# Kernel optimization log

Measured on AMD Instinct MI355X. Metric: run time of the kernel, lower is better.

Reference implementation:

```python
import jax, jax.numpy as jnp
import numpy as np

NEG_SLOPE = 0.2  # DGL GATConv default leaky_relu slope


def gat_conv(x, src, dst, W, attn_l, attn_r, bias, res_W):
    """DGL GATConv (eval mode, residual=True with linear res_fc, bias).
    x: [N, F_in]; src/dst: [E]; W: [F_in, H*D]; attn_l/r: [H, D];
    bias: [H*D]; res_W: [F_in, H*D]. Returns [N, H, D]."""
    N = x.shape[0]
    H, D = attn_l.shape
    feat = (x @ W).reshape(N, H, D)
    el = jnp.sum(feat * attn_l, axis=-1)  # [N, H]
    er = jnp.sum(feat * attn_r, axis=-1)  # [N, H]
    e = jax.nn.leaky_relu(el[src] + er[dst], NEG_SLOPE)  # [E, H]
    # edge softmax over incoming edges of each dst node (numerically stable)
    m = jnp.full((N, H), -jnp.inf, dtype=e.dtype).at[dst].max(e)
    ex = jnp.exp(e - m[dst])
    s = jnp.zeros((N, H), dtype=e.dtype).at[dst].add(ex)
    alpha = ex / s[dst]  # [E, H]
    # scatter-aggregate messages alpha * feat[src] into dst
    rst = jnp.zeros((N, H, D), dtype=x.dtype).at[dst].add(alpha[:, :, None] * feat[src])
    rst = rst + (x @ res_W).reshape(N, H, D) + bias.reshape(1, H, D)
    return rst


def setup_inputs() -> dict:
    key = jax.random.key(0)
    N, E, F_IN, HID, OUT, H = 20000, 320000, 128, 128, 128, 4
    ks = jax.random.split(key, 32)
    ki = iter(range(32))

    def rn(shape, scale=0.05):
        return jax.random.normal(ks[next(ki)], shape, dtype=jnp.float32) * scale

    inp = {
        "n_feat": jax.random.normal(ks[next(ki)], (N, F_IN), dtype=jnp.float32),
        "src": jax.random.randint(ks[next(ki)], (E,), 0, N, dtype=jnp.int32),
        "dst": jax.random.randint(ks[next(ki)], (E,), 0, N, dtype=jnp.int32),
        # input GATConv: F_IN -> H x HID
        "W0": rn((F_IN, H * HID)), "al0": rn((H, HID)), "ar0": rn((H, HID)),
        "b0": rn((H * HID,)), "rW0": rn((F_IN, H * HID)),
        "DW0": rn((H * HID, HID)), "Db0": rn((HID,)),
        # middle GATConv: HID -> H x HID
        "W1": rn((HID, H * HID)), "al1": rn((H, HID)), "ar1": rn((H, HID)),
        "b1": rn((H * HID,)), "rW1": rn((HID, H * HID)),
        "DW1": rn((H * HID, HID)), "Db1": rn((HID,)),
        # output GATConv: HID -> H x OUT
        "W2": rn((HID, H * OUT)), "al2": rn((H, OUT)), "ar2": rn((H, OUT)),
        "b2": rn((H * OUT,)), "rW2": rn((HID, H * OUT)),
    }
    return inp


def reference(n_feat, src, dst,
              W0, al0, ar0, b0, rW0, DW0, Db0,
              W1, al1, ar1, b1, rW1, DW1, Db1,
              W2, al2, ar2, b2, rW2):
    N = n_feat.shape[0]
    relu = jax.nn.relu
    # input GAT block
    h = relu(gat_conv(n_feat, src, dst, W0, al0, ar0, b0, rW0))  # [N, H, HID]
    h = relu(h.reshape(N, -1) @ DW0 + Db0)                        # [N, HID]
    # middle GAT block
    h = relu(gat_conv(h, src, dst, W1, al1, ar1, b1, rW1))
    h = relu(h.reshape(N, -1) @ DW1 + Db1)
    # output GAT + head-mean + graph max pooling (single graph)
    h = relu(gat_conv(h, src, dst, W2, al2, ar2, b2, rW2))        # [N, H, OUT]
    h = relu(jnp.mean(h, axis=-2))                                 # [N, OUT]
    return jnp.max(h, axis=0, keepdims=True)                       # [1, OUT]
```

## Files before the change

### kernel.cpp

```cpp
#include <hip/hip_runtime.h>
#include <hip/hip_bf16.h>


typedef __attribute__((ext_vector_type(8))) short bf16x8;
typedef __attribute__((ext_vector_type(4))) float f32x4;
typedef __hip_bfloat16 bf16_t;

#define NEG_SLOPE 0.2f

__device__ __forceinline__ unsigned int pack_bf16(float lo, float hi) {
  return (((unsigned int)__bfloat16_as_ushort(__float2bfloat16(hi))) << 16) |
         (unsigned int)__bfloat16_as_ushort(__float2bfloat16(lo));
}

__device__ __forceinline__ float leaky_exp(float e) {
  e = (e > 0.f) ? e : NEG_SLOPE * e;
  return __expf(e);
}

__device__ __forceinline__ void gload_lds16(const void* g, void* l) {
  __builtin_amdgcn_global_load_lds(
      (const __attribute__((address_space(1))) void*)g,
      (__attribute__((address_space(3))) void*)l, 16, 0, 0);
}

__global__ __launch_bounds__(256) void mega_prep(
    const float* __restrict__ W0, const float* __restrict__ rW0,
    const float* __restrict__ W1, const float* __restrict__ rW1,
    const float* __restrict__ W2, const float* __restrict__ rW2,
    const float* __restrict__ DW0, const float* __restrict__ DW1,
    const float* __restrict__ al0, const float* __restrict__ ar0,
    const float* __restrict__ al1, const float* __restrict__ ar1,
    const float* __restrict__ al2, const float* __restrict__ ar2,
    const float* __restrict__ n_feat, bf16_t* __restrict__ wts,
    float* __restrict__ ALR, bf16_t* __restrict__ xbf,
    int* __restrict__ counts, float* __restrict__ partials, int N) {
  __shared__ float tile[32][33];
  int b = blockIdx.x, tid = threadIdx.x;
  int r = tid >> 5, c = tid & 31;

  if (b < 384) {
    int mat = b >> 6;
    int t = b & 63;
    int kt = t >> 4, nt = t & 15;
    int L = mat >> 1, isR = mat & 1;
    const float* S = (L == 0) ? (isR ? rW0 : W0)
                   : (L == 1) ? (isR ? rW1 : W1) : (isR ? rW2 : W2);
    bf16_t* D = wts + L * 131072 + isR * 65536;
#pragma unroll
    for (int rr = 0; rr < 4; rr++)
      tile[r + rr * 8][c] = S[(kt * 32 + r + rr * 8) * 512 + nt * 32 + c];
    __syncthreads();
#pragma unroll
    for (int rr = 0; rr < 4; rr++)
      D[(nt * 32 + r + rr * 8) * 128 + kt * 32 + c] =
          __float2bfloat16(tile[c][r + rr * 8]);
  } else if (b < 512) {
    int i = b - 384;
    int mat = i >> 6;
    int t = i & 63;
    int kt = t & 15, nt = t >> 4;
    const float* S = mat ? DW1 : DW0;
    bf16_t* D = wts + 393216 + mat * 65536;
#pragma unroll
    for (int rr = 0; rr < 4; rr++)
      tile[r + rr * 8][c] = S[(kt * 32 + r + rr * 8) * 128 + nt * 32 + c];
    __syncthreads();
#pragma unroll
    for (int rr = 0; rr < 4; rr++)
      D[(nt * 32 + r + rr * 8) * 512 + kt * 32 + c] =
          __float2bfloat16(tile[c][r + rr * 8]);
  } else if (b < 524) {
    int idx = (b - 512) * 256 + tid;
    if (idx < 3072) {
      int L = idx >> 10;
      int k = (idx >> 3) & 127;
      int cc = idx & 7;
      int h = cc & 3;
      const float* W = (L == 0) ? W0 : (L == 1) ? W1 : W2;
      const float* a = (cc < 4) ? ((L == 0) ? al0 : (L == 1) ? al1 : al2)
                                : ((L == 0) ? ar0 : (L == 1) ? ar1 : ar2);
      float s = 0.f;
      for (int d = 0; d < 128; d++) s += W[k * 512 + h * 128 + d] * a[h * 128 + d];
      ALR[idx] = s;
    }
  } else if (b < 3024) {
    int i = ((b - 524) * 256 + tid) * 4;
    if (i < N * 128) {
      float4 v = *(const float4*)(n_feat + i);
      xbf[i + 0] = __float2bfloat16(v.x);
      xbf[i + 1] = __float2bfloat16(v.y);
      xbf[i + 2] = __float2bfloat16(v.z);
      xbf[i + 3] = __float2bfloat16(v.w);
    }
  } else {
    for (int i = tid; i < N; i += 256) counts[i] = 0;
    for (int i = tid; i < 64 * 128; i += 256) partials[i] = 0.f;
  }
}

template <bool COUNT>
__global__ __launch_bounds__(256) void gemm128el(
    const bf16_t* __restrict__ A, const bf16_t* __restrict__ Bt,
    const float* __restrict__ ALRl, bf16_t* __restrict__ featB,
    bf16_t* __restrict__ resB,
    float* __restrict__ el, float* __restrict__ er, int M, int K,
    const int* __restrict__ dst, int* __restrict__ counts, int E) {
  __shared__ bf16_t As[128 * 64];
  __shared__ bf16_t Bs[128 * 64];
  int tid = threadIdx.x;
  int rowBase = blockIdx.y * 128;

  if (COUNT && blockIdx.x == 9) {
    int stride = gridDim.y * 256;
    for (int i = blockIdx.y * 256 + tid; i < E; i += stride)
      atomicAdd(&counts[dst[i]], 1);
    return;
  }

  if (blockIdx.x == 8) {
    float* sALR = (float*)As;
#pragma unroll
    for (int j = 0; j < 4; j++) sALR[tid * 4 + j] = ALRl[tid * 4 + j];
    __syncthreads();
    int row = rowBase + (tid >> 1);
    int half = tid & 1;
    if (row < M) {
      const bf16_t* xr = A + (size_t)row * K + half * 64;
      float s[8] = {};
#pragma unroll
      for (int g = 0; g < 8; g++) {
        bf16x8 v = *(const bf16x8*)(xr + g * 8);
#pragma unroll
        for (int e = 0; e < 8; e++) {
          float f = __uint_as_float(((unsigned int)(unsigned short)v[e]) << 16);
          const float* Ak = sALR + (half * 64 + g * 8 + e) * 8;
#pragma unroll
          for (int cc = 0; cc < 8; cc++) s[cc] += f * Ak[cc];
        }
      }
#pragma unroll
      for (int cc = 0; cc < 8; cc++) s[cc] += __shfl_xor(s[cc], 1);
      if (half == 0)
        *(float4*)(el + row * 4) = make_float4(s[0], s[1], s[2], s[3]);
      else
        *(float4*)(er + row * 4) = make_float4(s[4], s[5], s[6], s[7]);
    }
    return;
  }

  int lane = tid & 63, wave = tid >> 6;
  int q = lane >> 4, r16 = lane & 15;
  int wm = (wave >> 1) * 64, wn = (wave & 1) * 64;
  int colBase = blockIdx.x * 128;
  bf16_t* Cb = (colBase < 512) ? featB : resB;
  int colOff = (colBase < 512) ? colBase : colBase - 512;

  f32x4 acc[4][4] = {};

  for (int k0 = 0; k0 < K; k0 += 64) {
#pragma unroll
    for (int p = 0; p < 4; p++) {
      int slotb = (wave * 4 + p) * 64;
      int s = slotb + lane;
      int r = s >> 3;
      int c = (s & 7) ^ (r & 7);
      int gr = rowBase + r;
      if (gr > M - 1) gr = M - 1;
      gload_lds16(A + (size_t)gr * K + k0 + c * 8, (char*)As + (size_t)slotb * 16);
      gload_lds16(Bt + (size_t)(colBase + r) * K + k0 + c * 8,
                  (char*)Bs + (size_t)slotb * 16);
    }
    __syncthreads();
#pragma unroll
    for (int ks = 0; ks < 64; ks += 32) {
      int koff = ks >> 3;
      bf16x8 af[4], bfr[4];
#pragma unroll
      for (int i = 0; i < 4; i++) {
        int R = wm + i * 16 + r16;
        int slot = R * 8 + ((q + koff) ^ (R & 7));
        af[i] = *(const bf16x8*)((const char*)As + (size_t)slot * 16);
      }
#pragma unroll
      for (int j = 0; j < 4; j++) {
        int R = wn + j * 16 + r16;
        int slot = R * 8 + ((q + koff) ^ (R & 7));
        bfr[j] = *(const bf16x8*)((const char*)Bs + (size_t)slot * 16);
      }
#pragma unroll
      for (int i = 0; i < 4; i++)
#pragma unroll
        for (int j = 0; j < 4; j++)
          acc[i][j] = __builtin_amdgcn_mfma_f32_16x16x32_bf16(af[i], bfr[j], acc[i][j], 0, 0, 0);
    }
    __syncthreads();
  }

  int odd = lane & 1;
  int colb0 = r16 & ~1;
#pragma unroll
  for (int i = 0; i < 4; i++) {
#pragma unroll
    for (int r = 0; r < 4; r++) {
      int row = rowBase + wm + i * 16 + q * 4 + r;
#pragma unroll
      for (int jp = 0; jp < 2; jp++) {
        float a0 = acc[i][2 * jp][r];
        float a1 = acc[i][2 * jp + 1][r];
        float p0 = __shfl_xor(a0, 1);
        float p1 = __shfl_xor(a1, 1);
        float lo = odd ? p1 : a0;
        float hi = odd ? a1 : p0;
        int col = colOff + wn + (2 * jp + odd) * 16 + colb0;
        if (row < M)
          *(unsigned int*)(Cb + (size_t)row * 512 + col) = pack_bf16(lo, hi);
      }
    }
  }
}

__global__ __launch_bounds__(256) void mfma_gemm64(
    const bf16_t* __restrict__ A, const bf16_t* __restrict__ Bt,
    const float* __restrict__ bias, bf16_t* __restrict__ C,
    int M, int ldc, int K) {
  __shared__ bf16_t As[64 * 64];
  __shared__ bf16_t Bs[64 * 64];
  int tid = threadIdx.x;
  int lane = tid & 63, wave = tid >> 6;
  int q = lane >> 4, r16 = lane & 15;
  int wm = (wave >> 1) * 32, wn = (wave & 1) * 32;
  int rowBase = blockIdx.y * 64, colBase = blockIdx.x * 64;

  f32x4 acc[2][2] = {};

  for (int k0 = 0; k0 < K; k0 += 64) {
#pragma unroll
    for (int p = 0; p < 2; p++) {
      int slotb = (wave * 2 + p) * 64;
      int s = slotb + lane;
      int r = s >> 3;
      int c = (s & 7) ^ (r & 7);
      int gr = rowBase + r;
      if (gr > M - 1) gr = M - 1;
      gload_lds16(A + (size_t)gr * K + k0 + c * 8, (char*)As + (size_t)slotb * 16);
      gload_lds16(Bt + (size_t)(colBase + r) * K + k0 + c * 8,
                  (char*)Bs + (size_t)slotb * 16);
    }
    __syncthreads();
#pragma unroll
    for (int ks = 0; ks < 64; ks += 32) {
      int koff = ks >> 3;
      bf16x8 af[2], bfr[2];
#pragma unroll
      for (int i = 0; i < 2; i++) {
        int R = wm + i * 16 + r16;
        int slot = R * 8 + ((q + koff) ^ (R & 7));
        af[i] = *(const bf16x8*)((const char*)As + (size_t)slot * 16);
      }
#pragma unroll
      for (int j = 0; j < 2; j++) {
        int R = wn + j * 16 + r16;
        int slot = R * 8 + ((q + koff) ^ (R & 7));
        bfr[j] = *(const bf16x8*)((const char*)Bs + (size_t)slot * 16);
      }
#pragma unroll
      for (int i = 0; i < 2; i++)
#pragma unroll
        for (int j = 0; j < 2; j++)
          acc[i][j] = __builtin_amdgcn_mfma_f32_16x16x32_bf16(af[i], bfr[j], acc[i][j], 0, 0, 0);
    }
    __syncthreads();
  }

  int odd = lane & 1;
  int colb0 = r16 & ~1;
#pragma unroll
  for (int i = 0; i < 2; i++) {
#pragma unroll
    for (int r = 0; r < 4; r++) {
      int row = rowBase + wm + i * 16 + q * 4 + r;
      float a0 = acc[i][0][r];
      float a1 = acc[i][1][r];
      float p0 = __shfl_xor(a0, 1);
      float p1 = __shfl_xor(a1, 1);
      float lo = odd ? p1 : a0;
      float hi = odd ? a1 : p0;
      int col = colBase + wn + odd * 16 + colb0;
      if (row < M) {
        float o0 = fmaxf(lo + bias[col], 0.f);
        float o1 = fmaxf(hi + bias[col + 1], 0.f);
        *(unsigned int*)(C + (size_t)row * ldc + col) = pack_bf16(o0, o1);
      }
    }
  }
}

__global__ __launch_bounds__(1024) void scan_kernel(const int* __restrict__ counts,
                                                    int* __restrict__ row_ptr,
                                                    int* __restrict__ cursor, int N) {
  __shared__ int sums[1024];
  int t = threadIdx.x;
  int chunk = (N + 1023) / 1024;
  int begin = t * chunk;
  int end = begin + chunk;
  if (end > N) end = N;
  int s = 0;
  for (int i = begin; i < end; i++) s += counts[i];
  sums[t] = s;
  __syncthreads();
  for (int off = 1; off < 1024; off <<= 1) {
    int v = (t >= off) ? sums[t - off] : 0;
    __syncthreads();
    sums[t] += v;
    __syncthreads();
  }
  int run = (t == 0) ? 0 : sums[t - 1];
  for (int i = begin; i < end; i++) {
    row_ptr[i] = run;
    cursor[i] = run;
    run += counts[i];
  }
  if (t == 1023) row_ptr[N] = sums[1023];
}

__global__ __launch_bounds__(256) void scatter_w_kernel(
    const int* __restrict__ src, const int* __restrict__ dst,
    int* __restrict__ cursor, int* __restrict__ edge_src,
    int* __restrict__ edge_dst, const float* __restrict__ el,
    const float* __restrict__ er, float* __restrict__ wcsr, int E) {
  int i = blockIdx.x * blockDim.x + threadIdx.x;
  if (i < E) {
    int s = src[i];
    int d = dst[i];
    int pos = atomicAdd(&cursor[d], 1);
    edge_src[pos] = s;
    edge_dst[pos] = d;
    float4 elv = *(const float4*)(el + s * 4);
    float4 erv = *(const float4*)(er + d * 4);
    float4 w;
    w.x = leaky_exp(elv.x + erv.x);
    w.y = leaky_exp(elv.y + erv.y);
    w.z = leaky_exp(elv.z + erv.z);
    w.w = leaky_exp(elv.w + erv.w);
    *(float4*)(wcsr + (size_t)pos * 4) = w;
  }
}

__global__ __launch_bounds__(256) void w_pass_kernel(
    const int* __restrict__ edge_src, const int* __restrict__ edge_dst,
    const float* __restrict__ el, const float* __restrict__ er,
    float* __restrict__ wcsr, int E) {
  int p = blockIdx.x * blockDim.x + threadIdx.x;
  if (p < E) {
    int s = edge_src[p];
    int d = edge_dst[p];
    float4 elv = *(const float4*)(el + s * 4);
    float4 erv = *(const float4*)(er + d * 4);
    float4 w;
    w.x = leaky_exp(elv.x + erv.x);
    w.y = leaky_exp(elv.y + erv.y);
    w.z = leaky_exp(elv.z + erv.z);
    w.w = leaky_exp(elv.w + erv.w);
    *(float4*)(wcsr + (size_t)p * 4) = w;
  }
}

template <bool POOL>
__global__ __launch_bounds__(256) void gat_agg_kernel(
    const bf16_t* __restrict__ featB,
    const bf16_t* __restrict__ resB,
    const float* __restrict__ wcsr,
    const float* __restrict__ bias, const int* __restrict__ row_ptr,
    const int* __restrict__ edge_src, bf16_t* __restrict__ out,
    float* __restrict__ partials, int N) {
  __shared__ float accL[4][64][8];
  __shared__ float ssumL[4][4];
  int n = blockIdx.x;
  int tid = threadIdx.x;
  int wave = tid >> 6, lane = tid & 63;
  int hh = lane >> 4;
  int start = row_ptr[n];
  int deg = row_ptr[n + 1] - start;

  float acc[8] = {};
  float ssum = 0.f;
  const bf16_t* fbase = featB + (size_t)lane * 8;
  for (int i = wave; i < deg; i += 4) {
    int p = start + i;
    int s = edge_src[p];
    float wv = wcsr[(size_t)p * 4 + hh];
    ssum += wv;
    uint4 f = *(const uint4*)(fbase + (size_t)s * 512);
    unsigned int u[4] = {f.x, f.y, f.z, f.w};
#pragma unroll
    for (int j = 0; j < 4; j++) {
      acc[2 * j] += wv * __uint_as_float(u[j] << 16);
      acc[2 * j + 1] += wv * __uint_as_float(u[j] & 0xffff0000u);
    }
  }
  *(float4*)&accL[wave][lane][0] = make_float4(acc[0], acc[1], acc[2], acc[3]);
  *(float4*)&accL[wave][lane][4] = make_float4(acc[4], acc[5], acc[6], acc[7]);
  if ((lane & 15) == 0) ssumL[wave][hh] = ssum;
  __syncthreads();

  int d = tid * 2;
  int l = d >> 3, j = d & 7;
  float a0 = 0.f, a1 = 0.f;
#pragma unroll
  for (int w = 0; w < 4; w++) {
    a0 += accL[w][l][j];
    a1 += accL[w][l][j + 1];
  }
  int h = tid >> 6;
  float ssum4 = ssumL[0][h] + ssumL[1][h] + ssumL[2][h] + ssumL[3][h];
  float inv = (deg > 0) ? 1.f / ssum4 : 0.f;
  unsigned int ru = *(const unsigned int*)(resB + (size_t)n * 512 + d);
  float2 bv = *(const float2*)(bias + d);
  float o0 = fmaxf(a0 * inv + __uint_as_float(ru << 16) + bv.x, 0.f);
  float o1 = fmaxf(a1 * inv + __uint_as_float(ru & 0xffff0000u) + bv.y, 0.f);

  if (!POOL) {
    *(unsigned int*)(out + (size_t)n * 512 + d) = pack_bf16(o0, o1);
  } else {
    float2* red = (float2*)accL;
    __syncthreads();
    red[tid] = make_float2(o0, o1);
    __syncthreads();
    if (tid < 64) {
      float m0 = 0.25f * (red[tid].x + red[tid + 64].x + red[tid + 128].x + red[tid + 192].x);
      float m1 = 0.25f * (red[tid].y + red[tid + 64].y + red[tid + 128].y + red[tid + 192].y);
      float* slot = partials + (n & 63) * 128;
      atomicMax((int*)slot + 2 * tid, __float_as_int(m0));
      atomicMax((int*)slot + 2 * tid + 1, __float_as_int(m1));
    }
  }
}

__global__ __launch_bounds__(128) void pool_finish(const float* __restrict__ partials,
                                                   float* __restrict__ out) {
  int d = threadIdx.x;
  float m = 0.f;
#pragma unroll 8
  for (int s = 0; s < 64; s++) m = fmaxf(m, partials[s * 128 + d]);
  out[d] = m;
}

extern "C" void kernel_launch(void* const* d_in, const int* in_sizes, int n_in,
                              void* d_out, int out_size, void* d_ws, size_t ws_size,
                              hipStream_t stream) {
  const float* n_feat = (const float*)d_in[0];
  const int* src = (const int*)d_in[1];
  const int* dst = (const int*)d_in[2];
  const float* W0 = (const float*)d_in[3];
  const float* al0 = (const float*)d_in[4];
  const float* ar0 = (const float*)d_in[5];
  const float* b0 = (const float*)d_in[6];
  const float* rW0 = (const float*)d_in[7];
  const float* DW0 = (const float*)d_in[8];
  const float* Db0 = (const float*)d_in[9];
  const float* W1 = (const float*)d_in[10];
  const float* al1 = (const float*)d_in[11];
  const float* ar1 = (const float*)d_in[12];
  const float* b1 = (const float*)d_in[13];
  const float* rW1 = (const float*)d_in[14];
  const float* DW1 = (const float*)d_in[15];
  const float* Db1 = (const float*)d_in[16];
  const float* W2 = (const float*)d_in[17];
  const float* al2 = (const float*)d_in[18];
  const float* ar2 = (const float*)d_in[19];
  const float* b2 = (const float*)d_in[20];
  const float* rW2 = (const float*)d_in[21];

  const int N = in_sizes[0] / 128;
  const int E = in_sizes[1];

  bf16_t* xbf = (bf16_t*)d_ws;
  bf16_t* featB = xbf + (size_t)N * 128;
  bf16_t* resB = featB + (size_t)N * 512;
  bf16_t* outC = resB + (size_t)N * 512;
  bf16_t* denseD = outC + (size_t)N * 512;
  bf16_t* wts = denseD + (size_t)N * 128;
  float* ALR = (float*)(wts + 524288);
  float* el = ALR + 3072;
  float* er = el + (size_t)N * 4;
  float* partials = er + (size_t)N * 4;
  float* wcsr = partials + 64 * 128;
  int* counts = (int*)(wcsr + (size_t)E * 4);
  int* row_ptr = counts + N;
  int* cursor = row_ptr + (N + 1);
  int* edge_src = cursor + N;
  int* edge_dst = edge_src + E;

  bf16_t* FW0 = wts;
  bf16_t* FW1 = wts + 131072;
  bf16_t* FW2 = wts + 262144;
  bf16_t* DWt0 = wts + 393216;
  bf16_t* DWt1 = wts + 458752;

  mega_prep<<<3025, 256, 0, stream>>>(
      W0, rW0, W1, rW1, W2, rW2, DW0, DW1,
      al0, ar0, al1, ar1, al2, ar2,
      n_feat, wts, ALR, xbf, counts, partials, N);

  int nRow = (N + 127) / 128;
  dim3 gF0(10, nRow);
  dim3 gF(9, nRow);
  dim3 gD(2, (N + 63) / 64);
  int gE = (E + 255) / 256;

  gemm128el<true><<<gF0, 256, 0, stream>>>(xbf, FW0, ALR, featB, resB, el, er,
                                           N, 128, dst, counts, E);
  scan_kernel<<<1, 1024, 0, stream>>>(counts, row_ptr, cursor, N);
  scatter_w_kernel<<<gE, 256, 0, stream>>>(src, dst, cursor, edge_src, edge_dst,
                                           el, er, wcsr, E);

  gat_agg_kernel<false><<<N, 256, 0, stream>>>(featB, resB, wcsr, b0, row_ptr,
                                               edge_src, outC, nullptr, N);
  mfma_gemm64<<<gD, 256, 0, stream>>>(outC, DWt0, Db0, denseD, N, 128, 512);
  gemm128el<false><<<gF, 256, 0, stream>>>(denseD, FW1, ALR + 1024, featB, resB,
                                           el, er, N, 128, nullptr, nullptr, 0);
  w_pass_kernel<<<gE, 256, 0, stream>>>(edge_src, edge_dst, el, er, wcsr, E);
  gat_agg_kernel<false><<<N, 256, 0, stream>>>(featB, resB, wcsr, b1, row_ptr,
                                               edge_src, outC, nullptr, N);
  mfma_gemm64<<<gD, 256, 0, stream>>>(outC, DWt1, Db1, denseD, N, 128, 512);
  gemm128el<false><<<gF, 256, 0, stream>>>(denseD, FW2, ALR + 2048, featB, resB,
                                           el, er, N, 128, nullptr, nullptr, 0);
  w_pass_kernel<<<gE, 256, 0, stream>>>(edge_src, edge_dst, el, er, wcsr, E);
  gat_agg_kernel<true><<<N, 256, 0, stream>>>(featB, resB, wcsr, b2, row_ptr,
                                              edge_src, nullptr, partials, N);
  pool_finish<<<1, 128, 0, stream>>>(partials, (float*)d_out);
}
```

Before: 424.1 us.

## Fuse all GAT stages into one persistent cooperative kernel with grid syncs

Replaces the sequence of about fourteen separate kernel launches with a single cooperative persistent kernel. Each stage (prep, feature GEMM, CSR build, edge weights, aggregation, dense GEMM, pooling) becomes a device phase separated by grid.sync, and blocks grid-stride over tiles or nodes. GEMM tiles shrink from 128x128 to 64x64 so the fixed grid has enough work. This removes launch gaps and tail effects, but adds grid-wide barrier cost, caps occupancy at four blocks per CU, and has each block walk many nodes serially in the aggregation phase. The host also queries device properties and occupancy on every call.

Measured after the change: 1.466 ms. 246% more time.

```diff
diff --git a/kernel.cpp b/kernel.cpp
--- a/kernel.cpp
+++ b/kernel.cpp
@@ -1,5 +1,8 @@
 #include <hip/hip_runtime.h>
+#include <hip/hip_cooperative_groups.h>
 #include <hip/hip_bf16.h>
+
+namespace cg = cooperative_groups;
 
 
 typedef __attribute__((ext_vector_type(8))) short bf16x8;
@@ -18,201 +21,111 @@
   return __expf(e);
 }
 
-__device__ __forceinline__ void gload_lds16(const void* g, void* l) {
+__device__ __forceinline__ void gld16(const void* g, void* l) {
   __builtin_amdgcn_global_load_lds(
       (const __attribute__((address_space(1))) void*)g,
       (__attribute__((address_space(3))) void*)l, 16, 0, 0);
 }
 
-__global__ __launch_bounds__(256) void mega_prep(
-    const float* __restrict__ W0, const float* __restrict__ rW0,
-    const float* __restrict__ W1, const float* __restrict__ rW1,
-    const float* __restrict__ W2, const float* __restrict__ rW2,
-    const float* __restrict__ DW0, const float* __restrict__ DW1,
-    const float* __restrict__ al0, const float* __restrict__ ar0,
-    const float* __restrict__ al1, const float* __restrict__ ar1,
-    const float* __restrict__ al2, const float* __restrict__ ar2,
-    const float* __restrict__ n_feat, bf16_t* __restrict__ wts,
-    float* __restrict__ ALR, bf16_t* __restrict__ xbf,
-    int* __restrict__ counts, float* __restrict__ partials, int N) {
-  __shared__ float tile[32][33];
-  int b = blockIdx.x, tid = threadIdx.x;
-  int r = tid >> 5, c = tid & 31;
-
-  if (b < 384) {
-    int mat = b >> 6;
-    int t = b & 63;
-    int kt = t >> 4, nt = t & 15;
-    int L = mat >> 1, isR = mat & 1;
-    const float* S = (L == 0) ? (isR ? rW0 : W0)
-                   : (L == 1) ? (isR ? rW1 : W1) : (isR ? rW2 : W2);
-    bf16_t* D = wts + L * 131072 + isR * 65536;
-#pragma unroll
-    for (int rr = 0; rr < 4; rr++)
-      tile[r + rr * 8][c] = S[(kt * 32 + r + rr * 8) * 512 + nt * 32 + c];
-    __syncthreads();
-#pragma unroll
-    for (int rr = 0; rr < 4; rr++)
-      D[(nt * 32 + r + rr * 8) * 128 + kt * 32 + c] =
-          __float2bfloat16(tile[c][r + rr * 8]);
-  } else if (b < 512) {
-    int i = b - 384;
-    int mat = i >> 6;
-    int t = i & 63;
-    int kt = t & 15, nt = t >> 4;
-    const float* S = mat ? DW1 : DW0;
-    bf16_t* D = wts + 393216 + mat * 65536;
-#pragma unroll
-    for (int rr = 0; rr < 4; rr++)
-      tile[r + rr * 8][c] = S[(kt * 32 + r + rr * 8) * 128 + nt * 32 + c];
-    __syncthreads();
-#pragma unroll
-    for (int rr = 0; rr < 4; rr++)
-      D[(nt * 32 + r + rr * 8) * 512 + kt * 32 + c] =
-          __float2bfloat16(tile[c][r + rr * 8]);
-  } else if (b < 524) {
-    int idx = (b - 512) * 256 + tid;
-    if (idx < 3072) {
-      int L = idx >> 10;
-      int k = (idx >> 3) & 127;
-      int cc = idx & 7;
-      int h = cc & 3;
-      const float* W = (L == 0) ? W0 : (L == 1) ? W1 : W2;
-      const float* a = (cc < 4) ? ((L == 0) ? al0 : (L == 1) ? al1 : al2)
-                                : ((L == 0) ? ar0 : (L == 1) ? ar1 : ar2);
-      float s = 0.f;
-      for (int d = 0; d < 128; d++) s += W[k * 512 + h * 128 + d] * a[h * 128 + d];
-      ALR[idx] = s;
-    }
-  } else if (b < 3024) {
-    int i = ((b - 524) * 256 + tid) * 4;
-    if (i < N * 128) {
-      float4 v = *(const float4*)(n_feat + i);
-      xbf[i + 0] = __float2bfloat16(v.x);
-      xbf[i + 1] = __float2bfloat16(v.y);
-      xbf[i + 2] = __float2bfloat16(v.z);
-      xbf[i + 3] = __float2bfloat16(v.w);
-    }
-  } else {
-    for (int i = tid; i < N; i += 256) counts[i] = 0;
-    for (int i = tid; i < 64 * 128; i += 256) partials[i] = 0.f;
-  }
-}
-
-template <bool COUNT>
-__global__ __launch_bounds__(256) void gemm128el(
+__device__ __forceinline__ void gemm_fused_phase(
     const bf16_t* __restrict__ A, const bf16_t* __restrict__ Bt,
     const float* __restrict__ ALRl, bf16_t* __restrict__ featB,
-    bf16_t* __restrict__ resB,
-    float* __restrict__ el, float* __restrict__ er, int M, int K,
-    const int* __restrict__ dst, int* __restrict__ counts, int E) {
-  __shared__ bf16_t As[128 * 64];
-  __shared__ bf16_t Bs[128 * 64];
-  int tid = threadIdx.x;
-  int rowBase = blockIdx.y * 128;
-
-  if (COUNT && blockIdx.x == 9) {
-    int stride = gridDim.y * 256;
-    for (int i = blockIdx.y * 256 + tid; i < E; i += stride)
-      atomicAdd(&counts[dst[i]], 1);
-    return;
-  }
-
-  if (blockIdx.x == 8) {
-    float* sALR = (float*)As;
-#pragma unroll
-    for (int j = 0; j < 4; j++) sALR[tid * 4 + j] = ALRl[tid * 4 + j];
-    __syncthreads();
-    int row = rowBase + (tid >> 1);
-    int half = tid & 1;
-    if (row < M) {
-      const bf16_t* xr = A + (size_t)row * K + half * 64;
-      float s[8] = {};
-#pragma unroll
-      for (int g = 0; g < 8; g++) {
-        bf16x8 v = *(const bf16x8*)(xr + g * 8);
-#pragma unroll
-        for (int e = 0; e < 8; e++) {
-          float f = __uint_as_float(((unsigned int)(unsigned short)v[e]) << 16);
-          const float* Ak = sALR + (half * 64 + g * 8 + e) * 8;
-#pragma unroll
-          for (int cc = 0; cc < 8; cc++) s[cc] += f * Ak[cc];
-        }
-      }
-#pragma unroll
-      for (int cc = 0; cc < 8; cc++) s[cc] += __shfl_xor(s[cc], 1);
-      if (half == 0)
-        *(float4*)(el + row * 4) = make_float4(s[0], s[1], s[2], s[3]);
-      else
-        *(float4*)(er + row * 4) = make_float4(s[4], s[5], s[6], s[7]);
-    }
-    return;
-  }
-
+    bf16_t* __restrict__ resB, float* __restrict__ el, float* __restrict__ er,
+    int M, int K, bf16_t* As, bf16_t* Bs, int tid, int bid, int nB) {
+  int nRow = (M + 63) / 64;
+  int tiles = 17 * nRow;
   int lane = tid & 63, wave = tid >> 6;
   int q = lane >> 4, r16 = lane & 15;
-  int wm = (wave >> 1) * 64, wn = (wave & 1) * 64;
-  int colBase = blockIdx.x * 128;
-  bf16_t* Cb = (colBase < 512) ? featB : resB;
-  int colOff = (colBase < 512) ? colBase : colBase - 512;
-
-  f32x4 acc[4][4] = {};
-
-  for (int k0 = 0; k0 < K; k0 += 64) {
-#pragma unroll
-    for (int p = 0; p < 4; p++) {
-      int slotb = (wave * 4 + p) * 64;
-      int s = slotb + lane;
-      int r = s >> 3;
-      int c = (s & 7) ^ (r & 7);
-      int gr = rowBase + r;
-      if (gr > M - 1) gr = M - 1;
-      gload_lds16(A + (size_t)gr * K + k0 + c * 8, (char*)As + (size_t)slotb * 16);
-      gload_lds16(Bt + (size_t)(colBase + r) * K + k0 + c * 8,
-                  (char*)Bs + (size_t)slotb * 16);
-    }
-    __syncthreads();
-#pragma unroll
-    for (int ks = 0; ks < 64; ks += 32) {
-      int koff = ks >> 3;
-      bf16x8 af[4], bfr[4];
-#pragma unroll
-      for (int i = 0; i < 4; i++) {
-        int R = wm + i * 16 + r16;
-        int slot = R * 8 + ((q + koff) ^ (R & 7));
-        af[i] = *(const bf16x8*)((const char*)As + (size_t)slot * 16);
-      }
-#pragma unroll
-      for (int j = 0; j < 4; j++) {
-        int R = wn + j * 16 + r16;
-        int slot = R * 8 + ((q + koff) ^ (R & 7));
-        bfr[j] = *(const bf16x8*)((const char*)Bs + (size_t)slot * 16);
-      }
-#pragma unroll
-      for (int i = 0; i < 4; i++)
-#pragma unroll
-        for (int j = 0; j < 4; j++)
-          acc[i][j] = __builtin_amdgcn_mfma_f32_16x16x32_bf16(af[i], bfr[j], acc[i][j], 0, 0, 0);
-    }
-    __syncthreads();
-  }
-
-  int odd = lane & 1;
-  int colb0 = r16 & ~1;
-#pragma unroll
-  for (int i = 0; i < 4; i++) {
-#pragma unroll
-    for (int r = 0; r < 4; r++) {
-      int row = rowBase + wm + i * 16 + q * 4 + r;
-#pragma unroll
-      for (int jp = 0; jp < 2; jp++) {
-        float a0 = acc[i][2 * jp][r];
-        float a1 = acc[i][2 * jp + 1][r];
-        float p0 = __shfl_xor(a0, 1);
-        float p1 = __shfl_xor(a1, 1);
-        float lo = odd ? p1 : a0;
-        float hi = odd ? a1 : p0;
-        int col = colOff + wn + (2 * jp + odd) * 16 + colb0;
+  int wm = (wave >> 1) * 32, wn = (wave & 1) * 32;
+  for (int t = bid; t < tiles; t += nB) {
+    int bx = t / nRow, by = t % nRow;
+    int rowBase = by * 64;
+    if (bx == 16) {
+      float* sALR = (float*)As;
+      for (int j = tid; j < 1024; j += 256) sALR[j] = ALRl[j];
+      __syncthreads();
+      int row = rowBase + (tid >> 2);
+      int q4 = tid & 3;
+      if (row < M) {
+        const bf16_t* xr = A + (size_t)row * K + q4 * 32;
+        float s[8] = {};
+#pragma unroll
+        for (int g = 0; g < 4; g++) {
+          bf16x8 v = *(const bf16x8*)(xr + g * 8);
+#pragma unroll
+          for (int e = 0; e < 8; e++) {
+            float f = __uint_as_float(((unsigned int)(unsigned short)v[e]) << 16);
+            const float* Ak = sALR + (q4 * 32 + g * 8 + e) * 8;
+#pragma unroll
+            for (int cc = 0; cc < 8; cc++) s[cc] += f * Ak[cc];
+          }
+        }
+#pragma unroll
+        for (int cc = 0; cc < 8; cc++) {
+          s[cc] += __shfl_xor(s[cc], 1);
+          s[cc] += __shfl_xor(s[cc], 2);
+        }
+        if (q4 == 0)
+          *(float4*)(el + row * 4) = make_float4(s[0], s[1], s[2], s[3]);
+        else if (q4 == 1)
+          *(float4*)(er + row * 4) = make_float4(s[4], s[5], s[6], s[7]);
+      }
+      __syncthreads();
+      continue;
+    }
+    int colBase = bx * 64;
+    bf16_t* Cb = (colBase < 512) ? featB : resB;
+    int colOff = (colBase < 512) ? colBase : colBase - 512;
+    f32x4 acc[2][2] = {};
+    for (int k0 = 0; k0 < K; k0 += 64) {
+#pragma unroll
+      for (int p = 0; p < 2; p++) {
+        int slotb = (wave * 2 + p) * 64;
+        int s = slotb + lane;
+        int r = s >> 3;
+        int c = (s & 7) ^ (r & 7);
+        int gr = rowBase + r;
+        if (gr > M - 1) gr = M - 1;
+        gld16(A + (size_t)gr * K + k0 + c * 8, (char*)As + (size_t)slotb * 16);
+        gld16(Bt + (size_t)(colBase + r) * K + k0 + c * 8,
+              (char*)Bs + (size_t)slotb * 16);
+      }
+      __syncthreads();
+#pragma unroll
+      for (int ks = 0; ks < 64; ks += 32) {
+        int koff = ks >> 3;
+        bf16x8 af[2], bfr[2];
+#pragma unroll
+        for (int i = 0; i < 2; i++) {
+          int R = wm + i * 16 + r16;
+          int slot = R * 8 + ((q + koff) ^ (R & 7));
+          af[i] = *(const bf16x8*)((const char*)As + (size_t)slot * 16);
+        }
+#pragma unroll
+        for (int j = 0; j < 2; j++) {
+          int R = wn + j * 16 + r16;
+          int slot = R * 8 + ((q + koff) ^ (R & 7));
+          bfr[j] = *(const bf16x8*)((const char*)Bs + (size_t)slot * 16);
+        }
+#pragma unroll
+        for (int i = 0; i < 2; i++)
+#pragma unroll
+          for (int j = 0; j < 2; j++)
+            acc[i][j] = __builtin_amdgcn_mfma_f32_16x16x32_bf16(af[i], bfr[j], acc[i][j], 0, 0, 0);
+      }
+      __syncthreads();
+    }
+    int odd = lane & 1;
+    int colb0 = r16 & ~1;
+#pragma unroll
+    for (int i = 0; i < 2; i++) {
+#pragma unroll
+      for (int rr = 0; rr < 4; rr++) {
+        int row = rowBase + wm + i * 16 + q * 4 + rr;
+        float a0 = acc[i][0][rr], a1 = acc[i][1][rr];
+        float p0 = __shfl_xor(a0, 1), p1 = __shfl_xor(a1, 1);
+        float lo = odd ? p1 : a0, hi = odd ? a1 : p0;
+        int col = colOff + wn + odd * 16 + colb0;
         if (row < M)
           *(unsigned int*)(Cb + (size_t)row * 512 + col) = pack_bf16(lo, hi);
       }
@@ -220,117 +133,288 @@
   }
 }
 
-__global__ __launch_bounds__(256) void mfma_gemm64(
+__device__ __forceinline__ void dense_phase(
     const bf16_t* __restrict__ A, const bf16_t* __restrict__ Bt,
     const float* __restrict__ bias, bf16_t* __restrict__ C,
-    int M, int ldc, int K) {
+    int M, int K, bf16_t* As, bf16_t* Bs, int tid, int bid, int nB) {
+  int nRow = (M + 63) / 64;
+  int tiles = 2 * nRow;
+  int lane = tid & 63, wave = tid >> 6;
+  int q = lane >> 4, r16 = lane & 15;
+  int wm = (wave >> 1) * 32, wn = (wave & 1) * 32;
+  for (int t = bid; t < tiles; t += nB) {
+    int bx = t / nRow, by = t % nRow;
+    int rowBase = by * 64, colBase = bx * 64;
+    f32x4 acc[2][2] = {};
+    for (int k0 = 0; k0 < K; k0 += 64) {
+#pragma unroll
+      for (int p = 0; p < 2; p++) {
+        int slotb = (wave * 2 + p) * 64;
+        int s = slotb + lane;
+        int r = s >> 3;
+        int c = (s & 7) ^ (r & 7);
+        int gr = rowBase + r;
+        if (gr > M - 1) gr = M - 1;
+        gld16(A + (size_t)gr * K + k0 + c * 8, (char*)As + (size_t)slotb * 16);
+        gld16(Bt + (size_t)(colBase + r) * K + k0 + c * 8,
+              (char*)Bs + (size_t)slotb * 16);
+      }
+      __syncthreads();
+#pragma unroll
+      for (int ks = 0; ks < 64; ks += 32) {
+        int koff = ks >> 3;
+        bf16x8 af[2], bfr[2];
+#pragma unroll
+        for (int i = 0; i < 2; i++) {
+          int R = wm + i * 16 + r16;
+          int slot = R * 8 + ((q + koff) ^ (R & 7));
+          af[i] = *(const bf16x8*)((const char*)As + (size_t)slot * 16);
+        }
+#pragma unroll
+        for (int j = 0; j < 2; j++) {
+          int R = wn + j * 16 + r16;
+          int slot = R * 8 + ((q + koff) ^ (R & 7));
+          bfr[j] = *(const bf16x8*)((const char*)Bs + (size_t)slot * 16);
+        }
+#pragma unroll
+        for (int i = 0; i < 2; i++)
+#pragma unroll
+          for (int j = 0; j < 2; j++)
+            acc[i][j] = __builtin_amdgcn_mfma_f32_16x16x32_bf16(af[i], bfr[j], acc[i][j], 0, 0, 0);
+      }
+      __syncthreads();
+    }
+    int odd = lane & 1;
+    int colb0 = r16 & ~1;
+#pragma unroll
+    for (int i = 0; i < 2; i++) {
+#pragma unroll
+      for (int rr = 0; rr < 4; rr++) {
+        int row = rowBase + wm + i * 16 + q * 4 + rr;
+        float a0 = acc[i][0][rr], a1 = acc[i][1][rr];
+        float p0 = __shfl_xor(a0, 1), p1 = __shfl_xor(a1, 1);
+        float lo = odd ? p1 : a0, hi = odd ? a1 : p0;
+        int col = colBase + wn + odd * 16 + colb0;
+        if (row < M) {
+          float o0 = fmaxf(lo + bias[col], 0.f);
+          float o1 = fmaxf(hi + bias[col + 1], 0.f);
+          *(unsigned int*)(C + (size_t)row * 128 + col) = pack_bf16(o0, o1);
+        }
+      }
+    }
+  }
+}
+
+__device__ __forceinline__ void w_phase(
+    const int* __restrict__ edge_src, const int* __restrict__ edge_dst,
+    const float* __restrict__ el, const float* __restrict__ er,
+    float* __restrict__ wcsr, int E, int tid, int bid, int nB) {
+  for (int p = bid * 256 + tid; p < E; p += nB * 256) {
+    int s = edge_src[p];
+    int d = edge_dst[p];
+    float4 elv = *(const float4*)(el + s * 4);
+    float4 erv = *(const float4*)(er + d * 4);
+    float4 w;
+    w.x = leaky_exp(elv.x + erv.x);
+    w.y = leaky_exp(elv.y + erv.y);
+    w.z = leaky_exp(elv.z + erv.z);
+    w.w = leaky_exp(elv.w + erv.w);
+    *(float4*)(wcsr + (size_t)p * 4) = w;
+  }
+}
+
+__device__ __forceinline__ void agg_phase(
+    const bf16_t* __restrict__ featB, const bf16_t* __restrict__ resB,
+    const float* __restrict__ wcsr, const float* __restrict__ bias,
+    const int* __restrict__ row_ptr, const int* __restrict__ edge_src,
+    bf16_t* __restrict__ out, float* __restrict__ partials, int N, int pool,
+    bf16_t* As, bf16_t* Bs, int tid, int bid, int nB) {
+  float(*accL)[64][8] = (float(*)[64][8])As;
+  float(*ssumL)[4] = (float(*)[4])Bs;
+  float2* red = (float2*)((char*)Bs + 128);
+  int wave = tid >> 6, lane = tid & 63;
+  int hh = lane >> 4;
+  for (int n = bid; n < N; n += nB) {
+    int start = row_ptr[n];
+    int deg = row_ptr[n + 1] - start;
+    float acc[8] = {};
+    float ssum = 0.f;
+    const bf16_t* fbase = featB + (size_t)lane * 8;
+    for (int i = wave; i < deg; i += 4) {
+      int p = start + i;
+      int s = edge_src[p];
+      float wv = wcsr[(size_t)p * 4 + hh];
+      ssum += wv;
+      uint4 f = *(const uint4*)(fbase + (size_t)s * 512);
+      unsigned int u[4] = {f.x, f.y, f.z, f.w};
+#pragma unroll
+      for (int j = 0; j < 4; j++) {
+        acc[2 * j] += wv * __uint_as_float(u[j] << 16);
+        acc[2 * j + 1] += wv * __uint_as_float(u[j] & 0xffff0000u);
+      }
+    }
+    *(float4*)&accL[wave][lane][0] = make_float4(acc[0], acc[1], acc[2], acc[3]);
+    *(float4*)&accL[wave][lane][4] = make_float4(acc[4], acc[5], acc[6], acc[7]);
+    if ((lane & 15) == 0) ssumL[wave][hh] = ssum;
+    __syncthreads();
+    int d = tid * 2;
+    int l = d >> 3, j = d & 7;
+    float a0 = 0.f, a1 = 0.f;
+#pragma unroll
+    for (int w = 0; w < 4; w++) {
+      a0 += accL[w][l][j];
+      a1 += accL[w][l][j + 1];
+    }
+    int h = tid >> 6;
+    float ssum4 = ssumL[0][h] + ssumL[1][h] + ssumL[2][h] + ssumL[3][h];
+    float inv = (deg > 0) ? 1.f / ssum4 : 0.f;
+    unsigned int ru = *(const unsigned int*)(resB + (size_t)n * 512 + d);
+    float2 bv = *(const float2*)(bias + d);
+    float o0 = fmaxf(a0 * inv + __uint_as_float(ru << 16) + bv.x, 0.f);
+    float o1 = fmaxf(a1 * inv + __uint_as_float(ru & 0xffff0000u) + bv.y, 0.f);
+    if (!pool) {
+      *(unsigned int*)(out + (size_t)n * 512 + d) = pack_bf16(o0, o1);
+      __syncthreads();
+    } else {
+      __syncthreads();
+      red[tid] = make_float2(o0, o1);
+      __syncthreads();
+      if (tid < 64) {
+        float m0 = 0.25f * (red[tid].x + red[tid + 64].x + red[tid + 128].x + red[tid + 192].x);
+        float m1 = 0.25f * (red[tid].y + red[tid + 64].y + red[tid + 128].y + red[tid + 192].y);
+        float* slot = partials + (n & 63) * 128;
+        atomicMax((int*)slot + 2 * tid, __float_as_int(m0));
+        atomicMax((int*)slot + 2 * tid + 1, __float_as_int(m1));
+      }
+      __syncthreads();
+    }
+  }
+}
+
+__global__ __launch_bounds__(256, 4) void fused_all(
+    const float* n_feat, const int* src, const int* dst,
+    const float* W0, const float* al0, const float* ar0, const float* b0,
+    const float* rW0, const float* DW0, const float* Db0,
+    const float* W1, const float* al1, const float* ar1, const float* b1,
+    const float* rW1, const float* DW1, const float* Db1,
+    const float* W2, const float* al2, const float* ar2, const float* b2,
+    const float* rW2,
+    bf16_t* xbf, bf16_t* featB, bf16_t* resB, bf16_t* outC, bf16_t* denseD,
+    bf16_t* wts, float* ALR, float* el, float* er, float* partials,
+    float* wcsr, int* counts, int* row_ptr, int* cursor,
+    int* edge_src, int* edge_dst, float* d_out_f, int N, int E) {
+  cg::grid_group grid = cg::this_grid();
   __shared__ bf16_t As[64 * 64];
   __shared__ bf16_t Bs[64 * 64];
   int tid = threadIdx.x;
-  int lane = tid & 63, wave = tid >> 6;
-  int q = lane >> 4, r16 = lane & 15;
-  int wm = (wave >> 1) * 32, wn = (wave & 1) * 32;
-  int rowBase = blockIdx.y * 64, colBase = blockIdx.x * 64;
-
-  f32x4 acc[2][2] = {};
-
-  for (int k0 = 0; k0 < K; k0 += 64) {
-#pragma unroll
-    for (int p = 0; p < 2; p++) {
-      int slotb = (wave * 2 + p) * 64;
-      int s = slotb + lane;
-      int r = s >> 3;
-      int c = (s & 7) ^ (r & 7);
-      int gr = rowBase + r;
-      if (gr > M - 1) gr = M - 1;
-      gload_lds16(A + (size_t)gr * K + k0 + c * 8, (char*)As + (size_t)slotb * 16);
-      gload_lds16(Bt + (size_t)(colBase + r) * K + k0 + c * 8,
-                  (char*)Bs + (size_t)slotb * 16);
-    }
+  int bid = blockIdx.x;
+  int nB = gridDim.x;
+
+  bf16_t* FW0 = wts;
+  bf16_t* FW1 = wts + 131072;
+  bf16_t* FW2 = wts + 262144;
+  bf16_t* DWt0 = wts + 393216;
+  bf16_t* DWt1 = wts + 458752;
+
+  {
+    float(*tile)[33] = (float(*)[33])As;
+    int r = tid >> 5, c = tid & 31;
+    int convCnt = ((N * 128 / 4) + 255) / 256;
+    int total = 524 + convCnt + 1;
+    for (int b = bid; b < total; b += nB) {
+      if (b < 384) {
+        int mat = b >> 6, t = b & 63;
+        int kt = t >> 4, nt = t & 15;
+        int L = mat >> 1, isR = mat & 1;
+        const float* S = (L == 0) ? (isR ? rW0 : W0)
+                       : (L == 1) ? (isR ? rW1 : W1) : (isR ? rW2 : W2);
+        bf16_t* D = wts + L * 131072 + isR * 65536;
+#pragma unroll
+        for (int rr = 0; rr < 4; rr++)
+          tile[r + rr * 8][c] = S[(kt * 32 + r + rr * 8) * 512 + nt * 32 + c];
+        __syncthreads();
+#pragma unroll
+        for (int rr = 0; rr < 4; rr++)
+          D[(nt * 32 + r + rr * 8) * 128 + kt * 32 + c] =
+              __float2bfloat16(tile[c][r + rr * 8]);
+      } else if (b < 512) {
+        int i = b - 384;
+        int mat = i >> 6, t = i & 63;
+        int kt = t & 15, nt = t >> 4;
+        const float* S = mat ? DW1 : DW0;
+        bf16_t* D = wts + 393216 + mat * 65536;
+#pragma unroll
+        for (int rr = 0; rr < 4; rr++)
+          tile[r + rr * 8][c] = S[(kt * 32 + r + rr * 8) * 128 + nt * 32 + c];
+        __syncthreads();
+#pragma unroll
+        for (int rr = 0; rr < 4; rr++)
+          D[(nt * 32 + r + rr * 8) * 512 + kt * 32 + c] =
+              __float2bfloat16(tile[c][r + rr * 8]);
+      } else if (b < 524) {
+        int idx = (b - 512) * 256 + tid;
+        if (idx < 3072) {
+          int L = idx >> 10;
+          int k = (idx >> 3) & 127;
+          int cc = idx & 7;
+          int h = cc & 3;
+          const float* W = (L == 0) ? W0 : (L == 1) ? W1 : W2;
+          const float* a = (cc < 4) ? ((L == 0) ? al0 : (L == 1) ? al1 : al2)
+                                    : ((L == 0) ? ar0 : (L == 1) ? ar1 : ar2);
+          float s = 0.f;
+          for (int d = 0; d < 128; d++)
+            s += W[k * 512 + h * 128 + d] * a[h * 128 + d];
+          ALR[idx] = s;
+        }
+      } else if (b < 524 + convCnt) {
+        int i = ((b - 524) * 256 + tid) * 4;
+        if (i < N * 128) {
+          float4 v = *(const float4*)(n_feat + i);
+          xbf[i + 0] = __float2bfloat16(v.x);
+          xbf[i + 1] = __float2bfloat16(v.y);
+          xbf[i + 2] = __float2bfloat16(v.z);
+          xbf[i + 3] = __float2bfloat16(v.w);
+        }
+      } else {
+        for (int i = tid; i < N; i += 256) counts[i] = 0;
+        for (int i = tid; i < 64 * 128; i += 256) partials[i] = 0.f;
+      }
+      __syncthreads();
+    }
+  }
+  grid.sync();
+
+  gemm_fused_phase(xbf, FW0, ALR, featB, resB, el, er, N, 128, As, Bs, tid, bid, nB);
+  for (int i = bid * 256 + tid; i < E; i += nB * 256) atomicAdd(&counts[dst[i]], 1);
+  grid.sync();
+
+  if (bid == 0) {
+    int* sums = (int*)As;
+    int chunk = (N + 255) / 256;
+    int begin = tid * chunk;
+    int end = begin + chunk;
+    if (end > N) end = N;
+    int s = 0;
+    for (int i = begin; i < end; i++) s += counts[i];
+    sums[tid] = s;
     __syncthreads();
-#pragma unroll
-    for (int ks = 0; ks < 64; ks += 32) {
-      int koff = ks >> 3;
-      bf16x8 af[2], bfr[2];
-#pragma unroll
-      for (int i = 0; i < 2; i++) {
-        int R = wm + i * 16 + r16;
-        int slot = R * 8 + ((q + koff) ^ (R & 7));
-        af[i] = *(const bf16x8*)((const char*)As + (size_t)slot * 16);
-      }
-#pragma unroll
-      for (int j = 0; j < 2; j++) {
-        int R = wn + j * 16 + r16;
-        int slot = R * 8 + ((q + koff) ^ (R & 7));
-        bfr[j] = *(const bf16x8*)((const char*)Bs + (size_t)slot * 16);
-      }
-#pragma unroll
-      for (int i = 0; i < 2; i++)
-#pragma unroll
-        for (int j = 0; j < 2; j++)
-          acc[i][j] = __builtin_amdgcn_mfma_f32_16x16x32_bf16(af[i], bfr[j], acc[i][j], 0, 0, 0);
-    }
-    __syncthreads();
-  }
-
-  int odd = lane & 1;
-  int colb0 = r16 & ~1;
-#pragma unroll
-  for (int i = 0; i < 2; i++) {
-#pragma unroll
-    for (int r = 0; r < 4; r++) {
-      int row = rowBase + wm + i * 16 + q * 4 + r;
-      float a0 = acc[i][0][r];
-      float a1 = acc[i][1][r];
-      float p0 = __shfl_xor(a0, 1);
-      float p1 = __shfl_xor(a1, 1);
-      float lo = odd ? p1 : a0;
-      float hi = odd ? a1 : p0;
-      int col = colBase + wn + odd * 16 + colb0;
-      if (row < M) {
-        float o0 = fmaxf(lo + bias[col], 0.f);
-        float o1 = fmaxf(hi + bias[col + 1], 0.f);
-        *(unsigned int*)(C + (size_t)row * ldc + col) = pack_bf16(o0, o1);
-      }
-    }
-  }
-}
-
-__global__ __launch_bounds__(1024) void scan_kernel(const int* __restrict__ counts,
-                                                    int* __restrict__ row_ptr,
-                                                    int* __restrict__ cursor, int N) {
-  __shared__ int sums[1024];
-  int t = threadIdx.x;
-  int chunk = (N + 1023) / 1024;
-  int begin = t * chunk;
-  int end = begin + chunk;
-  if (end > N) end = N;
-  int s = 0;
-  for (int i = begin; i < end; i++) s += counts[i];
-  sums[t] = s;
-  __syncthreads();
-  for (int off = 1; off < 1024; off <<= 1) {
-    int v = (t >= off) ? sums[t - off] : 0;
-    __syncthreads();
-    sums[t] += v;
-    __syncthreads();
-  }
-  int run = (t == 0) ? 0 : sums[t - 1];
-  for (int i = begin; i < end; i++) {
-    row_ptr[i] = run;
-    cursor[i] = run;
-    run += counts[i];
-  }
-  if (t == 1023) row_ptr[N] = sums[1023];
-}
-
-__global__ __launch_bounds__(256) void scatter_w_kernel(
-    const int* __restrict__ src, const int* __restrict__ dst,
-    int* __restrict__ cursor, int* __restrict__ edge_src,
-    int* __restrict__ edge_dst, const float* __restrict__ el,
-    const float* __restrict__ er, float* __restrict__ wcsr, int E) {
-  int i = blockIdx.x * blockDim.x + threadIdx.x;
-  if (i < E) {
+    for (int off = 1; off < 256; off <<= 1) {
+      int v = (tid >= off) ? sums[tid - off] : 0;
+      __syncthreads();
+      sums[tid] += v;
+      __syncthreads();
+    }
+    int run = (tid == 0) ? 0 : sums[tid - 1];
+    for (int i = begin; i < end; i++) {
+      row_ptr[i] = run;
+      cursor[i] = run;
+      run += counts[i];
+    }
+    if (tid == 255) row_ptr[N] = sums[255];
+  }
+  grid.sync();
+
+  for (int i = bid * 256 + tid; i < E; i += nB * 256) {
     int s = src[i];
     int d = dst[i];
     int pos = atomicAdd(&cursor[d], 1);
@@ -345,105 +429,34 @@
     w.w = leaky_exp(elv.w + erv.w);
     *(float4*)(wcsr + (size_t)pos * 4) = w;
   }
-}
-
-__global__ __launch_bounds__(256) void w_pass_kernel(
-    const int* __restrict__ edge_src, const int* __restrict__ edge_dst,
-    const float* __restrict__ el, const float* __restrict__ er,
-    float* __restrict__ wcsr, int E) {
-  int p = blockIdx.x * blockDim.x + threadIdx.x;
-  if (p < E) {
-    int s = edge_src[p];
-    int d = edge_dst[p];
-    float4 elv = *(const float4*)(el + s * 4);
-    float4 erv = *(const float4*)(er + d * 4);
-    float4 w;
-    w.x = leaky_exp(elv.x + erv.x);
-    w.y = leaky_exp(elv.y + erv.y);
-    w.z = leaky_exp(elv.z + erv.z);
-    w.w = leaky_exp(elv.w + erv.w);
-    *(float4*)(wcsr + (size_t)p * 4) = w;
-  }
-}
-
-template <bool POOL>
-__global__ __launch_bounds__(256) void gat_agg_kernel(
-    const bf16_t* __restrict__ featB,
-    const bf16_t* __restrict__ resB,
-    const float* __restrict__ wcsr,
-    const float* __restrict__ bias, const int* __restrict__ row_ptr,
-    const int* __restrict__ edge_src, bf16_t* __restrict__ out,
-    float* __restrict__ partials, int N) {
-  __shared__ float accL[4][64][8];
-  __shared__ float ssumL[4][4];
-  int n = blockIdx.x;
-  int tid = threadIdx.x;
-  int wave = tid >> 6, lane = tid & 63;
-  int hh = lane >> 4;
-  int start = row_ptr[n];
-  int deg = row_ptr[n + 1] - start;
-
-  float acc[8] = {};
-  float ssum = 0.f;
-  const bf16_t* fbase = featB + (size_t)lane * 8;
-  for (int i = wave; i < deg; i += 4) {
-    int p = start + i;
-    int s = edge_src[p];
-    float wv = wcsr[(size_t)p * 4 + hh];
-    ssum += wv;
-    uint4 f = *(const uint4*)(fbase + (size_t)s * 512);
-    unsigned int u[4] = {f.x, f.y, f.z, f.w};
-#pragma unroll
-    for (int j = 0; j < 4; j++) {
-      acc[2 * j] += wv * __uint_as_float(u[j] << 16);
-      acc[2 * j + 1] += wv * __uint_as_float(u[j] & 0xffff0000u);
-    }
-  }
-  *(float4*)&accL[wave][lane][0] = make_float4(acc[0], acc[1], acc[2], acc[3]);
-  *(float4*)&accL[wave][lane][4] = make_float4(acc[4], acc[5], acc[6], acc[7]);
-  if ((lane & 15) == 0) ssumL[wave][hh] = ssum;
-  __syncthreads();
-
-  int d = tid * 2;
-  int l = d >> 3, j = d & 7;
-  float a0 = 0.f, a1 = 0.f;
-#pragma unroll
-  for (int w = 0; w < 4; w++) {
-    a0 += accL[w][l][j];
-    a1 += accL[w][l][j + 1];
-  }
-  int h = tid >> 6;
-  float ssum4 = ssumL[0][h] + ssumL[1][h] + ssumL[2][h] + ssumL[3][h];
-  float inv = (deg > 0) ? 1.f / ssum4 : 0.f;
-  unsigned int ru = *(const unsigned int*)(resB + (size_t)n * 512 + d);
-  float2 bv = *(const float2*)(bias + d);
-  float o0 = fmaxf(a0 * inv + __uint_as_float(ru << 16) + bv.x, 0.f);
-  float o1 = fmaxf(a1 * inv + __uint_as_float(ru & 0xffff0000u) + bv.y, 0.f);
-
-  if (!POOL) {
-    *(unsigned int*)(out + (size_t)n * 512 + d) = pack_bf16(o0, o1);
-  } else {
-    float2* red = (float2*)accL;
-    __syncthreads();
-    red[tid] = make_float2(o0, o1);
-    __syncthreads();
-    if (tid < 64) {
-      float m0 = 0.25f * (red[tid].x + red[tid + 64].x + red[tid + 128].x + red[tid + 192].x);
-      float m1 = 0.25f * (red[tid].y + red[tid + 64].y + red[tid + 128].y + red[tid + 192].y);
-      float* slot = partials + (n & 63) * 128;
-      atomicMax((int*)slot + 2 * tid, __float_as_int(m0));
-      atomicMax((int*)slot + 2 * tid + 1, __float_as_int(m1));
-    }
-  }
-}
-
-__global__ __launch_bounds__(128) void pool_finish(const float* __restrict__ partials,
-                                                   float* __restrict__ out) {
-  int d = threadIdx.x;
-  float m = 0.f;
-#pragma unroll 8
-  for (int s = 0; s < 64; s++) m = fmaxf(m, partials[s * 128 + d]);
-  out[d] = m;
+  grid.sync();
+
+  agg_phase(featB, resB, wcsr, b0, row_ptr, edge_src, outC, partials, N, 0,
+            As, Bs, tid, bid, nB);
+  grid.sync();
+  dense_phase(outC, DWt0, Db0, denseD, N, 512, As, Bs, tid, bid, nB);
+  grid.sync();
+  gemm_fused_phase(denseD, FW1, ALR + 1024, featB, resB, el, er, N, 128, As, Bs, tid, bid, nB);
+  grid.sync();
+  w_phase(edge_src, edge_dst, el, er, wcsr, E, tid, bid, nB);
+  grid.sync();
+  agg_phase(featB, resB, wcsr, b1, row_ptr, edge_src, outC, partials, N, 0,
+            As, Bs, tid, bid, nB);
+  grid.sync();
+  dense_phase(outC, DWt1, Db1, denseD, N, 512, As, Bs, tid, bid, nB);
+  grid.sync();
+  gemm_fused_phase(denseD, FW2, ALR + 2048, featB, resB, el, er, N, 128, As, Bs, tid, bid, nB);
+  grid.sync();
+  w_phase(edge_src, edge_dst, el, er, wcsr, E, tid, bid, nB);
+  grid.sync();
+  agg_phase(featB, resB, wcsr, b2, row_ptr, edge_src, outC, partials, N, 1,
+            As, Bs, tid, bid, nB);
+  grid.sync();
+  if (bid == 0 && tid < 128) {
+    float m = 0.f;
+    for (int s = 0; s < 64; s++) m = fmaxf(m, partials[s * 128 + tid]);
+    d_out_f[tid] = m;
+  }
 }
 
 extern "C" void kernel_launch(void* const* d_in, const int* in_sizes, int n_in,
@@ -472,8 +485,8 @@
   const float* b2 = (const float*)d_in[20];
   const float* rW2 = (const float*)d_in[21];
 
-  const int N = in_sizes[0] / 128;
-  const int E = in_sizes[1];
+  int N = in_sizes[0] / 128;
+  int E = in_sizes[1];
 
   bf16_t* xbf = (bf16_t*)d_ws;
   bf16_t* featB = xbf + (size_t)N * 128;
@@ -491,43 +504,30 @@
   int* cursor = row_ptr + (N + 1);
   int* edge_src = cursor + N;
   int* edge_dst = edge_src + E;
-
-  bf16_t* FW0 = wts;
-  bf16_t* FW1 = wts + 131072;
-  bf16_t* FW2 = wts + 262144;
-  bf16_t* DWt0 = wts + 393216;
-  bf16_t* DWt1 = wts + 458752;
-
-  mega_prep<<<3025, 256, 0, stream>>>(
-      W0, rW0, W1, rW1, W2, rW2, DW0, DW1,
-      al0, ar0, al1, ar1, al2, ar2,
-      n_feat, wts, ALR, xbf, counts, partials, N);
-
-  int nRow = (N + 127) / 128;
-  dim3 gF0(10, nRow);
-  dim3 gF(9, nRow);
-  dim3 gD(2, (N + 63) / 64);
-  int gE = (E + 255) / 256;
-
-  gemm128el<true><<<gF0, 256, 0, stream>>>(xbf, FW0, ALR, featB, resB, el, er,
-                                           N, 128, dst, counts, E);
-  scan_kernel<<<1, 1024, 0, stream>>>(counts, row_ptr, cursor, N);
-  scatter_w_kernel<<<gE, 256, 0, stream>>>(src, dst, cursor, edge_src, edge_dst,
-                                           el, er, wcsr, E);
-
-  gat_agg_kernel<false><<<N, 256, 0, stream>>>(featB, resB, wcsr, b0, row_ptr,
-                                               edge_src, outC, nullptr, N);
-  mfma_gemm64<<<gD, 256, 0, stream>>>(outC, DWt0, Db0, denseD, N, 128, 512);
-  gemm128el<false><<<gF, 256, 0, stream>>>(denseD, FW1, ALR + 1024, featB, resB,
-                                           el, er, N, 128, nullptr, nullptr, 0);
-  w_pass_kernel<<<gE, 256, 0, stream>>>(edge_src, edge_dst, el, er, wcsr, E);
-  gat_agg_kernel<false><<<N, 256, 0, stream>>>(featB, resB, wcsr, b1, row_ptr,
-                                               edge_src, outC, nullptr, N);
-  mfma_gemm64<<<gD, 256, 0, stream>>>(outC, DWt1, Db1, denseD, N, 128, 512);
-  gemm128el<false><<<gF, 256, 0, stream>>>(denseD, FW2, ALR + 2048, featB, resB,
-                                           el, er, N, 128, nullptr, nullptr, 0);
-  w_pass_kernel<<<gE, 256, 0, stream>>>(edge_src, edge_dst, el, er, wcsr, E);
-  gat_agg_kernel<true><<<N, 256, 0, stream>>>(featB, resB, wcsr, b2, row_ptr,
-                                              edge_src, nullptr, partials, N);
-  pool_finish<<<1, 128, 0, stream>>>(partials, (float*)d_out);
-}
+  float* d_out_f = (float*)d_out;
+
+  void* args[] = {
+      (void*)&n_feat, (void*)&src, (void*)&dst,
+      (void*)&W0, (void*)&al0, (void*)&ar0, (void*)&b0, (void*)&rW0,
+      (void*)&DW0, (void*)&Db0,
+      (void*)&W1, (void*)&al1, (void*)&ar1, (void*)&b1, (void*)&rW1,
+      (void*)&DW1, (void*)&Db1,
+      (void*)&W2, (void*)&al2, (void*)&ar2, (void*)&b2, (void*)&rW2,
+      (void*)&xbf, (void*)&featB, (void*)&resB, (void*)&outC, (void*)&denseD,
+      (void*)&wts, (void*)&ALR, (void*)&el, (void*)&er, (void*)&partials,
+      (void*)&wcsr, (void*)&counts, (void*)&row_ptr, (void*)&cursor,
+      (void*)&edge_src, (void*)&edge_dst, (void*)&d_out_f, (void*)&N, (void*)&E};
+
+  int blocksPerCU = 0;
+  hipOccupancyMaxActiveBlocksPerMultiprocessor(&blocksPerCU, fused_all, 256, 0);
+  if (blocksPerCU < 1) blocksPerCU = 1;
+  hipDeviceProp_t prop;
+  int dev = 0;
+  hipGetDevice(&dev);
+  hipGetDeviceProperties(&prop, dev);
+  int grid = blocksPerCU * prop.multiProcessorCount;
+  if (grid < 64) grid = 64;
+
+  hipLaunchCooperativeKernel((const void*)fused_all, dim3(grid), dim3(256),
+                             args, 0, stream);
+}
```
